# Kernel tuning notes

Hardware: AMD Instinct MI355X
Metric: run time of the kernel (lower is better)

## Reference

```python
import jax, jax.numpy as jnp
import numpy as np

N_NODES = 100000   # destination-node segments for edge_softmax
N_GRAPHS = 128     # batched graphs for sum_edges readout
E = 1_600_000      # total edges (avg degree 16)
F = 64             # in_feats
NEG_SLOPE = 0.01   # torch LeakyReLU default


def setup_inputs() -> dict:
    key = jax.random.key(0)
    k1, k2, k3, k4 = jax.random.split(key, 4)
    edge_feats = jax.random.normal(k1, (E, F), jnp.float32)
    W = jax.random.normal(k2, (F, 1), jnp.float32) / np.sqrt(F)
    b = jnp.zeros((1,), jnp.float32)
    edge_dst = jnp.sort(jax.random.randint(k3, (E,), 0, N_NODES)).astype(jnp.int32)
    graph_ids = jnp.sort(jax.random.randint(k4, (E,), 0, N_GRAPHS)).astype(jnp.int32)
    return {"edge_feats": edge_feats, "W": W, "b": b,
            "edge_dst": edge_dst, "graph_ids": graph_ids}


def reference(edge_feats, W, b, edge_dst, graph_ids):
    # per-edge scalar score: Linear(F,1) + LeakyReLU
    s = jax.nn.leaky_relu(edge_feats @ W + b, negative_slope=NEG_SLOPE)[:, 0]  # [E]
    # edge_softmax: numerically-stable softmax over edges sharing a dst node
    m = jax.ops.segment_max(s, edge_dst, num_segments=N_NODES, indices_are_sorted=True)   # [N]
    ex = jnp.exp(s - m[edge_dst])                                                          # [E]
    den = jax.ops.segment_sum(ex, edge_dst, num_segments=N_NODES, indices_are_sorted=True) # [N]
    weights = (ex / den[edge_dst])[:, None]                                                # [E,1]
    # dgl.sum_edges(g, 'e', 'w'): per-graph weighted sum of edge features
    h_g_sum = jax.ops.segment_sum(edge_feats * weights, graph_ids,
                                  num_segments=N_GRAPHS, indices_are_sorted=True)          # [G,F]
    return h_g_sum, weights
```

## Files before the change

### kernel.cpp

```cpp
#include <hip/hip_runtime.h>
#include <math.h>

#define E_TOTAL 1600000
#define NN 100000
#define NG 128
#define FF 64
#define NGROUPS (E_TOTAL / 64)

__global__ __launch_bounds__(256) void init_kernel(float* den, float* hg) {
    int i = blockIdx.x * blockDim.x + threadIdx.x;
    if (i < NN) den[i] = 0.0f;
    if (i < NG * FF) hg[i] = 0.0f;
}

__global__ __launch_bounds__(256) void score_kernel(
        const float4* __restrict__ feats4, const float4* __restrict__ W4,
        const float* __restrict__ b, const int* __restrict__ dst,
        float* __restrict__ exbuf, float* __restrict__ den) {
    int tid  = blockIdx.x * blockDim.x + threadIdx.x;
    int lane = threadIdx.x & 63;
    int wave = tid >> 6;
    int nw   = (gridDim.x * blockDim.x) >> 6;
    int sub  = lane >> 4;
    int sl   = lane & 15;
    float4 w = W4[sl];
    float bias = b[0];
    for (int ebase = wave * 4; ebase < E_TOTAL; ebase += nw * 4) {
        int e = ebase + sub;
        float4 v = feats4[(size_t)e * 16 + sl];
        float dq = v.x * w.x + v.y * w.y + v.z * w.z + v.w * w.w;
        dq += __shfl_xor(dq, 1);
        dq += __shfl_xor(dq, 2);
        dq += __shfl_xor(dq, 4);
        dq += __shfl_xor(dq, 8);
        float ex = 0.0f; int d = -1;
        if (sl == 0) {
            float sv = dq + bias;
            sv = sv > 0.0f ? sv : 0.01f * sv;
            ex = __expf(sv);
            exbuf[e] = ex;
            d = dst[e];
        }
        float sp = __shfl_up(ex, 16); int dp = __shfl_up(d, 16);
        if (sub >= 1 && dp == d) ex += sp;
        sp = __shfl_up(ex, 32); dp = __shfl_up(d, 32);
        if (sub >= 2 && dp == d) ex += sp;
        int dn = __shfl_down(d, 16);
        if (sl == 0 && (sub == 3 || dn != d)) atomicAdd(&den[d], ex);
    }
}

__device__ __forceinline__ void flush_acc(float4& acc, int cur_g, int lane,
                                          float* __restrict__ hg) {
    acc.x += __shfl_xor(acc.x, 16); acc.y += __shfl_xor(acc.y, 16);
    acc.z += __shfl_xor(acc.z, 16); acc.w += __shfl_xor(acc.w, 16);
    acc.x += __shfl_xor(acc.x, 32); acc.y += __shfl_xor(acc.y, 32);
    acc.z += __shfl_xor(acc.z, 32); acc.w += __shfl_xor(acc.w, 32);
    if (lane < 16) {
        float* p = hg + cur_g * 64 + lane * 4;
        atomicAdd(p + 0, acc.x); atomicAdd(p + 1, acc.y);
        atomicAdd(p + 2, acc.z); atomicAdd(p + 3, acc.w);
    }
    acc.x = acc.y = acc.z = acc.w = 0.0f;
}

__global__ __launch_bounds__(256) void wsum_kernel(
        const float4* __restrict__ feats4, const float* __restrict__ exbuf,
        const float* __restrict__ den, const int* __restrict__ dst,
        const int* __restrict__ gid, float* __restrict__ wout,
        float* __restrict__ hg) {
    int tid  = blockIdx.x * blockDim.x + threadIdx.x;
    int lane = threadIdx.x & 63;
    int wave = tid >> 6;
    int nwaves = (gridDim.x * blockDim.x) >> 6;
    int gpw = (NGROUPS + nwaves - 1) / nwaves;
    int g0 = wave * gpw;
    if (g0 >= NGROUPS) return;
    int g1 = min(g0 + gpw, NGROUPS);
    int q = lane >> 4;
    float4 acc = {0.f, 0.f, 0.f, 0.f};
    int cur_g = -1;
    for (int grp = g0; grp < g1; ++grp) {
        int e = grp * 64 + lane;
        float w = exbuf[e] / den[dst[e]];
        wout[e] = w;
        int gg = gid[e];
        int gfirst = __builtin_amdgcn_readfirstlane(gg);
        bool uni = (__ballot(gg != gfirst) == 0ULL);
        const float4* frow = feats4 + (size_t)grp * 64 * 16;
        if (uni) {
            if (gfirst != cur_g) {
                if (cur_g >= 0) flush_acc(acc, cur_g, lane, hg);
                cur_g = gfirst;
            }
            #pragma unroll 4
            for (int it = 0; it < 16; ++it) {
                float we = __shfl(w, it * 4 + q);
                float4 v = frow[it * 64 + lane];
                acc.x += v.x * we; acc.y += v.y * we;
                acc.z += v.z * we; acc.w += v.w * we;
            }
        } else {
            int sl = lane & 15;
            for (int j = 0; j < 64; ++j) {
                int gj = __shfl(gg, j);
                if (gj != cur_g) {
                    if (cur_g >= 0) flush_acc(acc, cur_g, lane, hg);
                    cur_g = gj;
                }
                if (q == (j & 3)) {
                    float we = __shfl(w, j);
                    float4 v = frow[j * 16 + sl];
                    acc.x += v.x * we; acc.y += v.y * we;
                    acc.z += v.z * we; acc.w += v.w * we;
                }
            }
        }
    }
    if (cur_g >= 0) flush_acc(acc, cur_g, lane, hg);
}

extern "C" void kernel_launch(void* const* d_in, const int* in_sizes, int n_in,
                              void* d_out, int out_size, void* d_ws, size_t ws_size,
                              hipStream_t stream) {
    const float* feats = (const float*)d_in[0];
    const float* W     = (const float*)d_in[1];
    const float* b     = (const float*)d_in[2];
    const int*   dst   = (const int*)d_in[3];
    const int*   gid   = (const int*)d_in[4];

    float* out   = (float*)d_out;
    float* hg    = out;
    float* wout  = out + NG * FF;

    float* exbuf = (float*)d_ws;
    float* den   = exbuf + E_TOTAL;

    init_kernel<<<(NN + 255) / 256, 256, 0, stream>>>(den, hg);
    score_kernel<<<2048, 256, 0, stream>>>((const float4*)feats, (const float4*)W,
                                           b, dst, exbuf, den);
    wsum_kernel<<<1024, 256, 0, stream>>>((const float4*)feats, exbuf, den,
                                          dst, gid, wout, hg);
}
```

Before: 635.5 us.

## Fuse score and weighted-sum passes into one segment-aligned single-read kernel

Replaces the separate score and weighted-sum kernels with one kernel in which each wave owns a range of edges aligned to destination-segment boundaries. Because each segment is then handled by a single wave, the softmax denominator can be accumulated locally without atomics, and the feature sum can be scaled by the reciprocal denominator when the segment closes, so the 410MB feature matrix is read once instead of twice. A small fixup kernel then turns the stored exponentials into normalized weights using a per-node reciprocal. The cost is heavier per-wave bookkeeping for graph and segment boundaries and more registers. Like the original, it applies no max subtraction.

```diff
diff --git a/kernel.cpp b/kernel.cpp
--- a/kernel.cpp
+++ b/kernel.cpp
@@ -5,119 +5,168 @@
 #define NN 100000
 #define NG 128
 #define FF 64
-#define NGROUPS (E_TOTAL / 64)
 
-__global__ __launch_bounds__(256) void init_kernel(float* den, float* hg) {
+#define NWAVES 8192
+#define EPW ((E_TOTAL + NWAVES - 1) / NWAVES)
+
+__global__ __launch_bounds__(256) void init_hg(float* __restrict__ hg) {
     int i = blockIdx.x * blockDim.x + threadIdx.x;
-    if (i < NN) den[i] = 0.0f;
     if (i < NG * FF) hg[i] = 0.0f;
 }
 
-__global__ __launch_bounds__(256) void score_kernel(
+__device__ __forceinline__ int seg_start_from(const int* __restrict__ dst,
+                                              int X, int lane) {
+    if (X <= 0) return 0;
+    if (X >= E_TOTAL) return E_TOTAL;
+    for (;;) {
+        int e = X + lane;
+        bool bd = (e >= E_TOTAL) || (dst[e] != dst[e - 1]);
+        unsigned long long m = __ballot(bd);
+        if (m != 0ULL) {
+            int r = X + (__ffsll(m) - 1);
+            return r > E_TOTAL ? E_TOTAL : r;
+        }
+        X += 64;
+    }
+}
+
+__device__ __forceinline__ void hg_flush(float ax, float ay, float az, float aw,
+                                         int g, int lane, float* __restrict__ hg) {
+    ax += __shfl_xor(ax, 16); ay += __shfl_xor(ay, 16);
+    az += __shfl_xor(az, 16); aw += __shfl_xor(aw, 16);
+    ax += __shfl_xor(ax, 32); ay += __shfl_xor(ay, 32);
+    az += __shfl_xor(az, 32); aw += __shfl_xor(aw, 32);
+    if (lane < 16) {
+        float* p = hg + g * FF + lane * 4;
+        atomicAdd(p + 0, ax); atomicAdd(p + 1, ay);
+        atomicAdd(p + 2, az); atomicAdd(p + 3, aw);
+    }
+}
+
+#define CLOSE_SEG() do {                                                        \
+    if (cur_d >= 0) {                                                           \
+        float rden = 1.0f / den_cur;                                            \
+        if (lane == 0) rden_out[cur_d] = rden;                                  \
+        gx += sx * rden; gy += sy * rden; gz += sz * rden; gw += sw * rden;     \
+        if (nst > 0) hg_flush(s0x*rden, s0y*rden, s0z*rden, s0w*rden, st0g, lane, hg); \
+        if (nst > 1) hg_flush(s1x*rden, s1y*rden, s1z*rden, s1w*rden, st1g, lane, hg); \
+        if (nst > 2) hg_flush(s2x*rden, s2y*rden, s2z*rden, s2w*rden, st2g, lane, hg); \
+        nst = 0; sx = sy = sz = sw = 0.f; den_cur = 0.f; piece_any = false;     \
+    } } while (0)
+
+#define GRAPH_CHANGE(NEWG) do {                                                 \
+    if (cur_g >= 0) {                                                           \
+        if (piece_any) {                                                        \
+            if (nst == 0)      { s0x=sx; s0y=sy; s0z=sz; s0w=sw; st0g=cur_g; }  \
+            else if (nst == 1) { s1x=sx; s1y=sy; s1z=sz; s1w=sw; st1g=cur_g; }  \
+            else               { s2x=sx; s2y=sy; s2z=sz; s2w=sw; st2g=cur_g; }  \
+            nst++;                                                              \
+            sx = sy = sz = sw = 0.f; piece_any = false;                         \
+        }                                                                       \
+        hg_flush(gx, gy, gz, gw, cur_g, lane, hg);                              \
+        gx = gy = gz = gw = 0.f;                                                \
+    }                                                                           \
+    cur_g = (NEWG); } while (0)
+
+__global__ __launch_bounds__(256) void fused_kernel(
         const float4* __restrict__ feats4, const float4* __restrict__ W4,
         const float* __restrict__ b, const int* __restrict__ dst,
-        float* __restrict__ exbuf, float* __restrict__ den) {
+        const int* __restrict__ gid, float* __restrict__ exw,
+        float* __restrict__ rden_out, float* __restrict__ hg) {
     int tid  = blockIdx.x * blockDim.x + threadIdx.x;
     int lane = threadIdx.x & 63;
     int wave = tid >> 6;
-    int nw   = (gridDim.x * blockDim.x) >> 6;
     int sub  = lane >> 4;
     int sl   = lane & 15;
-    float4 w = W4[sl];
+
+    int Rb = wave * EPW;
+    if (Rb >= E_TOTAL) return;
+    int Re = Rb + EPW; if (Re > E_TOTAL) Re = E_TOTAL;
+
+    int s = seg_start_from(dst, Rb, lane);
+    int t = (Re >= E_TOTAL) ? E_TOTAL : seg_start_from(dst, Re, lane);
+    if (s >= t) return;
+
+    float4 wv = W4[sl];
     float bias = b[0];
-    for (int ebase = wave * 4; ebase < E_TOTAL; ebase += nw * 4) {
-        int e = ebase + sub;
-        float4 v = feats4[(size_t)e * 16 + sl];
-        float dq = v.x * w.x + v.y * w.y + v.z * w.z + v.w * w.w;
-        dq += __shfl_xor(dq, 1);
-        dq += __shfl_xor(dq, 2);
-        dq += __shfl_xor(dq, 4);
-        dq += __shfl_xor(dq, 8);
-        float ex = 0.0f; int d = -1;
-        if (sl == 0) {
-            float sv = dq + bias;
-            sv = sv > 0.0f ? sv : 0.01f * sv;
-            ex = __expf(sv);
-            exbuf[e] = ex;
-            d = dst[e];
+
+    int   cur_d = -1, cur_g = -1;
+    float den_cur = 0.0f;
+    bool  piece_any = false;
+    float sx=0.f, sy=0.f, sz=0.f, sw=0.f;
+    float gx=0.f, gy=0.f, gz=0.f, gw=0.f;
+    float s0x=0.f,s0y=0.f,s0z=0.f,s0w=0.f;
+    float s1x=0.f,s1y=0.f,s1z=0.f,s1w=0.f;
+    float s2x=0.f,s2y=0.f,s2z=0.f,s2w=0.f;
+    int   st0g=0, st1g=0, st2g=0, nst=0;
+
+    int e0 = s + sub;
+    int el = e0 < E_TOTAL ? e0 : E_TOTAL - 1;
+    float4 v = feats4[(size_t)el * 16 + sl];
+    int dcur = dst[el];
+    int gcur = gid[el];
+
+    for (int e4 = s; e4 < t; e4 += 4) {
+        float4 vn = v; int dn = dcur, gn = gcur;
+        int n4 = e4 + 4;
+        if (n4 < t) {
+            int en  = n4 + sub;
+            int eln = en < E_TOTAL ? en : E_TOTAL - 1;
+            vn = feats4[(size_t)eln * 16 + sl];
+            dn = dst[eln]; gn = gid[eln];
         }
-        float sp = __shfl_up(ex, 16); int dp = __shfl_up(d, 16);
-        if (sub >= 1 && dp == d) ex += sp;
-        sp = __shfl_up(ex, 32); dp = __shfl_up(d, 32);
-        if (sub >= 2 && dp == d) ex += sp;
-        int dn = __shfl_down(d, 16);
-        if (sl == 0 && (sub == 3 || dn != d)) atomicAdd(&den[d], ex);
-    }
-}
 
-__device__ __forceinline__ void flush_acc(float4& acc, int cur_g, int lane,
-                                          float* __restrict__ hg) {
-    acc.x += __shfl_xor(acc.x, 16); acc.y += __shfl_xor(acc.y, 16);
-    acc.z += __shfl_xor(acc.z, 16); acc.w += __shfl_xor(acc.w, 16);
-    acc.x += __shfl_xor(acc.x, 32); acc.y += __shfl_xor(acc.y, 32);
-    acc.z += __shfl_xor(acc.z, 32); acc.w += __shfl_xor(acc.w, 32);
-    if (lane < 16) {
-        float* p = hg + cur_g * 64 + lane * 4;
-        atomicAdd(p + 0, acc.x); atomicAdd(p + 1, acc.y);
-        atomicAdd(p + 2, acc.z); atomicAdd(p + 3, acc.w);
-    }
-    acc.x = acc.y = acc.z = acc.w = 0.0f;
-}
+        float dq = v.x*wv.x + v.y*wv.y + v.z*wv.z + v.w*wv.w;
+        dq += __shfl_xor(dq, 1); dq += __shfl_xor(dq, 2);
+        dq += __shfl_xor(dq, 4); dq += __shfl_xor(dq, 8);
+        float svv = dq + bias;
+        svv = svv > 0.0f ? svv : 0.01f * svv;
+        float ex = __expf(svv);
+        bool valid = (e4 + sub) < t;
+        if (!valid) ex = 0.0f;
+        if (sl == 0 && valid) exw[e4 + sub] = ex;
 
-__global__ __launch_bounds__(256) void wsum_kernel(
-        const float4* __restrict__ feats4, const float* __restrict__ exbuf,
-        const float* __restrict__ den, const int* __restrict__ dst,
-        const int* __restrict__ gid, float* __restrict__ wout,
-        float* __restrict__ hg) {
-    int tid  = blockIdx.x * blockDim.x + threadIdx.x;
-    int lane = threadIdx.x & 63;
-    int wave = tid >> 6;
-    int nwaves = (gridDim.x * blockDim.x) >> 6;
-    int gpw = (NGROUPS + nwaves - 1) / nwaves;
-    int g0 = wave * gpw;
-    if (g0 >= NGROUPS) return;
-    int g1 = min(g0 + gpw, NGROUPS);
-    int q = lane >> 4;
-    float4 acc = {0.f, 0.f, 0.f, 0.f};
-    int cur_g = -1;
-    for (int grp = g0; grp < g1; ++grp) {
-        int e = grp * 64 + lane;
-        float w = exbuf[e] / den[dst[e]];
-        wout[e] = w;
-        int gg = gid[e];
-        int gfirst = __builtin_amdgcn_readfirstlane(gg);
-        bool uni = (__ballot(gg != gfirst) == 0ULL);
-        const float4* frow = feats4 + (size_t)grp * 64 * 16;
-        if (uni) {
-            if (gfirst != cur_g) {
-                if (cur_g >= 0) flush_acc(acc, cur_g, lane, hg);
-                cur_g = gfirst;
-            }
-            #pragma unroll 4
-            for (int it = 0; it < 16; ++it) {
-                float we = __shfl(w, it * 4 + q);
-                float4 v = frow[it * 64 + lane];
-                acc.x += v.x * we; acc.y += v.y * we;
-                acc.z += v.z * we; acc.w += v.w * we;
-            }
+        bool diff = valid && ((dcur != cur_d) || (gcur != cur_g));
+        if (__ballot(diff) == 0ULL) {
+            sx += v.x * ex; sy += v.y * ex; sz += v.z * ex; sw += v.w * ex;
+            float q0 = ex + __shfl_xor(ex, 16);
+            den_cur += q0 + __shfl_xor(q0, 32);
+            piece_any = true;
         } else {
-            int sl = lane & 15;
-            for (int j = 0; j < 64; ++j) {
-                int gj = __shfl(gg, j);
-                if (gj != cur_g) {
-                    if (cur_g >= 0) flush_acc(acc, cur_g, lane, hg);
-                    cur_g = gj;
-                }
-                if (q == (j & 3)) {
-                    float we = __shfl(w, j);
-                    float4 v = frow[j * 16 + sl];
-                    acc.x += v.x * we; acc.y += v.y * we;
-                    acc.z += v.z * we; acc.w += v.w * we;
+            #pragma unroll
+            for (int j = 0; j < 4; ++j) {
+                if (e4 + j < t) {
+                    int   dj  = __shfl(dcur, j << 4);
+                    int   gj  = __shfl(gcur, j << 4);
+                    float exj = __shfl(ex,   j << 4);
+                    if (dj != cur_d) { CLOSE_SEG(); cur_d = dj; }
+                    if (gj != cur_g) { GRAPH_CHANGE(gj); }
+                    den_cur += exj;
+                    float m = (sub == j) ? ex : 0.0f;
+                    sx += v.x * m; sy += v.y * m; sz += v.z * m; sw += v.w * m;
+                    piece_any = true;
                 }
             }
         }
+        v = vn; dcur = dn; gcur = gn;
     }
-    if (cur_g >= 0) flush_acc(acc, cur_g, lane, hg);
+
+    CLOSE_SEG();
+    if (cur_g >= 0) hg_flush(gx, gy, gz, gw, cur_g, lane, hg);
+}
+
+__global__ __launch_bounds__(256) void fixup_kernel(
+        const int4* __restrict__ dst4, const float* __restrict__ rden,
+        float* __restrict__ wout) {
+    int i = blockIdx.x * blockDim.x + threadIdx.x;
+    if (i < E_TOTAL / 4) {
+        int4   d  = dst4[i];
+        float4 ex = ((const float4*)wout)[i];
+        float4 w;
+        w.x = ex.x * rden[d.x]; w.y = ex.y * rden[d.y];
+        w.z = ex.z * rden[d.z]; w.w = ex.w * rden[d.w];
+        ((float4*)wout)[i] = w;
+    }
 }
 
 extern "C" void kernel_launch(void* const* d_in, const int* in_sizes, int n_in,
@@ -129,16 +178,15 @@
     const int*   dst   = (const int*)d_in[3];
     const int*   gid   = (const int*)d_in[4];
 
-    float* out   = (float*)d_out;
-    float* hg    = out;
-    float* wout  = out + NG * FF;
+    float* out  = (float*)d_out;
+    float* hg   = out;
+    float* wout = out + NG * FF;
 
-    float* exbuf = (float*)d_ws;
-    float* den   = exbuf + E_TOTAL;
+    float* rden = (float*)d_ws;
 
-    init_kernel<<<(NN + 255) / 256, 256, 0, stream>>>(den, hg);
-    score_kernel<<<2048, 256, 0, stream>>>((const float4*)feats, (const float4*)W,
-                                           b, dst, exbuf, den);
-    wsum_kernel<<<1024, 256, 0, stream>>>((const float4*)feats, exbuf, den,
-                                          dst, gid, wout, hg);
+    init_hg<<<(NG * FF + 255) / 256, 256, 0, stream>>>(hg);
+    fused_kernel<<<NWAVES / 4, 256, 0, stream>>>(
+        (const float4*)feats, (const float4*)W, b, dst, gid, wout, rden, hg);
+    fixup_kernel<<<(E_TOTAL / 4 + 255) / 256, 256, 0, stream>>>(
+        (const int4*)dst, rden, wout);
 }
```

Result: faster. 569.6 us (-10.4%).
